# Kernel optimization log

Hardware: AMD Instinct MI355X
Metric: run time of the kernel (lower is better)

Reference implementation:

```python
import jax, jax.numpy as jnp
import numpy as np

HEADS = 8
DIM_HEAD = 64
DIM = 512
HIDDEN = HEADS * DIM_HEAD  # 512


def setup_inputs() -> dict:
    key = jax.random.key(0)
    k1, k2, k3, k4 = jax.random.split(key, 4)
    b, m, n = 4, 8, 512
    x = jax.random.normal(k1, (b, m, n, DIM), dtype=jnp.float32)
    pos_bias = jax.random.normal(k2, (HEADS, n, 16, 16), dtype=jnp.float32)
    # torch nn.Linear(dim, 3*hidden) weight is [3*hidden, dim]; we store the
    # transposed matmul form [dim, 3*hidden] for y = x @ W.
    w_qkv = jax.random.normal(k3, (DIM, 3 * HIDDEN), dtype=jnp.float32) * (DIM ** -0.5)
    w_out = jax.random.normal(k4, (HIDDEN, DIM), dtype=jnp.float32) * (HIDDEN ** -0.5)
    return {"x": x, "pos_bias": pos_bias, "w_qkv": w_qkv, "w_out": w_out}


def reference(x, pos_bias, w_qkv, w_out):
    b, m, n, _ = x.shape
    h, d = HEADS, DIM_HEAD
    scale = d ** -0.5
    qkv = jnp.einsum('bmnc,ce->bmne', x, w_qkv)  # [b,m,n,3*hidden]
    q, k, v = jnp.split(qkv, 3, axis=-1)
    # 'b m n (h d) -> (b m) h n d'
    def to_heads(t):
        return t.reshape(b * m, n, h, d).transpose(0, 2, 1, 3)
    q, k, v = to_heads(q), to_heads(k), to_heads(v)
    q = q * scale
    sim = jnp.einsum('bhid,bhjd->bhij', q, k)  # [(b*m), h, n, n]
    # pos_bias [h, n, p, q] -> mean over last two dims -> [h, n] -> broadcast [1,h,n,1]
    pb = pos_bias.mean(axis=(-2, -1))[None, :, :, None]
    sim = sim + pb
    sim = sim - jax.lax.stop_gradient(jnp.max(sim, axis=-1, keepdims=True))
    attn = jax.nn.softmax(sim, axis=-1)
    out = jnp.einsum('bhij,bhjd->bhid', attn, v)  # [(b*m), h, n, d]
    # '(b m) h n d -> b m n (h d)'
    out = out.transpose(0, 2, 1, 3).reshape(b, m, n, h * d)
    return jnp.einsum('bmne,ec->bmnc', out, w_out)
```

## Files before the change

### kernel.cpp

```cpp
#include <hip/hip_runtime.h>
#include <stdint.h>


typedef __attribute__((ext_vector_type(8))) short bf16x8;
typedef __attribute__((ext_vector_type(4))) float f32x4;
typedef __attribute__((ext_vector_type(4))) unsigned short us4;
typedef __attribute__((ext_vector_type(4))) float float4v;

__device__ __forceinline__ unsigned short f2b(float f) {
  union { float f; uint32_t u; } x; x.f = f;
  uint32_t r = x.u + 0x7fffu + ((x.u >> 16) & 1u);
  return (unsigned short)(r >> 16);
}

__device__ __forceinline__ uint32_t cvtpk(float lo, float hi) {
  uint32_t r;
  asm("v_cvt_pk_bf16_f32 %0, %1, %2" : "=v"(r) : "v"(lo), "v"(hi));
  return r;
}

__device__ __forceinline__ f32x4 mfma16(bf16x8 a, bf16x8 b, f32x4 c) {
  return __builtin_amdgcn_mfma_f32_16x16x32_bf16(a, b, c, 0, 0, 0);
}

__device__ __forceinline__ void gload_lds16(const unsigned short* g, unsigned short* l) {
  __builtin_amdgcn_global_load_lds(
      (const __attribute__((address_space(1))) unsigned int*)g,
      (__attribute__((address_space(3))) unsigned int*)l, 16, 0, 0);
}

__global__ __launch_bounds__(256) void cast_x_kernel(
    const float* __restrict__ src, unsigned short* __restrict__ dst) {
  size_t i = ((size_t)blockIdx.x * 256 + threadIdx.x) * 4;
  float4v v = *(const float4v*)(src + i);
  us4 o;
#pragma unroll
  for (int j = 0; j < 4; ++j) o[j] = f2b(v[j]);
  *(us4*)(dst + i) = o;
}

__global__ __launch_bounds__(256) void transpose_cast_kernel(
    const float* __restrict__ src, unsigned short* __restrict__ dst, int R, int C) {
  __shared__ float tile[64][65];
  const int tc0 = blockIdx.x * 64;
  const int tr0 = blockIdx.y * 64;
#pragma unroll
  for (int k2 = 0; k2 < 16; ++k2) {
    int idx = threadIdx.x + k2 * 256;
    int r = idx >> 6, c = idx & 63;
    tile[r][c] = src[(size_t)(tr0 + r) * C + tc0 + c];
  }
  __syncthreads();
#pragma unroll
  for (int k2 = 0; k2 < 16; ++k2) {
    int idx = threadIdx.x + k2 * 256;
    int c = idx >> 6, r = idx & 63;
    dst[(size_t)(tc0 + c) * R + tr0 + r] = f2b(tile[r][c]);
  }
}

__device__ __forceinline__ void gemm_core(
    const unsigned short* __restrict__ A, const unsigned short* __restrict__ Bt,
    int K, int r0, int c0, unsigned short* As, unsigned short* Bs,
    f32x4 (&acc)[4][4]) {
  const int tid = threadIdx.x;
  const int lane = tid & 63;
  const int wave = tid >> 6;
  const int wr = (wave >> 1) * 64;
  const int wc = (wave & 1) * 64;
  const int l15 = lane & 15;
  const int g = lane >> 4;
  const int lsw = l15 & 7;

#pragma unroll
  for (int m = 0; m < 4; ++m)
#pragma unroll
    for (int n = 0; n < 4; ++n) acc[m][n] = (f32x4){0.f, 0.f, 0.f, 0.f};

  for (int kt = 0; kt < K; kt += 64) {
#pragma unroll
    for (int i = 0; i < 4; ++i) {
      int chunk = tid + i * 256;
      int row = chunk >> 3;
      int csw = (chunk & 7) ^ (row & 7);
      gload_lds16(A + (size_t)(r0 + row) * K + kt + csw * 8, As + chunk * 8);
      gload_lds16(Bt + (size_t)(c0 + row) * K + kt + csw * 8, Bs + chunk * 8);
    }
    __syncthreads();
#pragma unroll
    for (int ks = 0; ks < 2; ++ks) {
      bf16x8 af[4], bfr[4];
      const int j = g + ks * 4;
      const int cj = (j ^ lsw) * 8;
#pragma unroll
      for (int m = 0; m < 4; ++m)
        af[m] = *(const bf16x8*)(As + (wr + m * 16 + l15) * 64 + cj);
#pragma unroll
      for (int n = 0; n < 4; ++n)
        bfr[n] = *(const bf16x8*)(Bs + (wc + n * 16 + l15) * 64 + cj);
#pragma unroll
      for (int m = 0; m < 4; ++m)
#pragma unroll
        for (int n = 0; n < 4; ++n) acc[m][n] = mfma16(af[m], bfr[n], acc[m][n]);
    }
    __syncthreads();
  }
}

__global__ __launch_bounds__(256) void gemm_qkv_kernel(
    const unsigned short* __restrict__ xb, const unsigned short* __restrict__ wqbT,
    unsigned short* __restrict__ qb, unsigned short* __restrict__ kb,
    unsigned short* __restrict__ vtb) {
  __shared__ unsigned short smem[16384];
  f32x4 acc[4][4];
  const int r0 = blockIdx.x * 128;
  const int c0 = blockIdx.y * 128;
  gemm_core(xb, wqbT, 512, r0, c0, smem, smem + 8192, acc);

  const int tid = threadIdx.x, lane = tid & 63, wave = tid >> 6;
  const int wr = (wave >> 1) * 64, wc = (wave & 1) * 64;
  const int l15 = lane & 15, g = lane >> 4;
  const int part = c0 >> 9;
  const float scl = (part == 0) ? 0.125f : 1.0f;

  if (part < 2) {
#pragma unroll
    for (int m = 0; m < 4; ++m) {
      int rbase = wr + m * 16 + 4 * g;
#pragma unroll
      for (int n = 0; n < 4; ++n) {
        int c = wc + n * 16 + l15;
        int c2 = c >> 3, ci = c & 7;
#pragma unroll
        for (int rr = 0; rr < 4; ++rr) {
          int r = rbase + rr;
          smem[r * 128 + ((c2 ^ (r & 15)) << 3) + ci] = f2b(acc[m][n][rr] * scl);
        }
      }
    }
    __syncthreads();
    unsigned short* dstb = (part == 0) ? qb : kb;
#pragma unroll
    for (int it = 0; it < 8; ++it) {
      int idx = tid + it * 256;
      int r = idx >> 4, c2 = idx & 15;
      bf16x8 v = *(const bf16x8*)(smem + r * 128 + ((c2 ^ (r & 15)) << 3));
      int e = c0 + c2 * 8;
      int rem = e & 511, h = rem >> 6, d = rem & 63;
      int ig = r0 + r;
      int bh = (ig >> 9) * 8 + h, i = ig & 511;
      *(bf16x8*)(dstb + ((size_t)bh * 512 + i) * 64 + d) = v;
    }
  } else {
#pragma unroll
    for (int m = 0; m < 4; ++m) {
      int rbase = wr + m * 16 + 4 * g;
      int r2 = rbase >> 3, rhalf = rbase & 7;
#pragma unroll
      for (int n = 0; n < 4; ++n) {
        int c = wc + n * 16 + l15;
        us4 v;
#pragma unroll
        for (int rr = 0; rr < 4; ++rr) v[rr] = f2b(acc[m][n][rr]);
        *(us4*)(smem + c * 128 + ((r2 ^ (c & 15)) << 3) + rhalf) = v;
      }
    }
    __syncthreads();
#pragma unroll
    for (int it = 0; it < 8; ++it) {
      int idx = tid + it * 256;
      int c = idx >> 4, r8 = idx & 15;
      bf16x8 v = *(const bf16x8*)(smem + c * 128 + ((r8 ^ (c & 15)) << 3));
      int e = c0 + c;
      int rem = e & 511, h = rem >> 6, d = rem & 63;
      int ig0 = r0 + r8 * 8;
      int bh = (ig0 >> 9) * 8 + h, i = ig0 & 511;
      *(bf16x8*)(vtb + ((size_t)bh * 64 + d) * 512 + i) = v;
    }
  }
}

__global__ __launch_bounds__(256) void gemm_out_kernel(
    const unsigned short* __restrict__ ao, const unsigned short* __restrict__ wobT,
    float* __restrict__ out) {
  __shared__ unsigned short smem[16384];
  f32x4 acc[4][4];
  const int r0 = blockIdx.x * 128;
  const int c0 = blockIdx.y * 128;
  gemm_core(ao, wobT, 512, r0, c0, smem, smem + 8192, acc);

  const int tid = threadIdx.x, lane = tid & 63, wave = tid >> 6;
  const int wr = (wave >> 1) * 64, wc = (wave & 1) * 64;
  const int l15 = lane & 15, g = lane >> 4;
#pragma unroll
  for (int m = 0; m < 4; ++m) {
    int i0g = r0 + wr + m * 16 + 4 * g;
#pragma unroll
    for (int n = 0; n < 4; ++n) {
      int e = c0 + wc + n * 16 + l15;
#pragma unroll
      for (int rr = 0; rr < 4; ++rr)
        out[(size_t)(i0g + rr) * 512 + e] = acc[m][n][rr];
    }
  }
}

__global__ __launch_bounds__(512, 4) void attn_kernel(
    const unsigned short* __restrict__ qb, const unsigned short* __restrict__ kb,
    const unsigned short* __restrict__ vtb, unsigned short* __restrict__ ao) {
  __shared__ unsigned short kbuf[2][8192];
  __shared__ unsigned short vbuf[2][8192];
  __shared__ unsigned short Ps[8][16][40];
  const int bh = blockIdx.x;
  const int qt = blockIdx.y;
  const int tid = threadIdx.x, lane = tid & 63, wave = tid >> 6;
  const int l15 = lane & 15, g = lane >> 4;
  const int qrow0 = qt * 128 + wave * 16;

  const unsigned short* Q = qb + ((size_t)bh * 512 + qrow0) * 64;
  const unsigned short* Kp = kb + (size_t)bh * 512 * 64;
  const unsigned short* Vt = vtb + (size_t)bh * 64 * 512;

  bf16x8 qf0 = *(const bf16x8*)(Q + l15 * 64 + g * 8);
  bf16x8 qf1 = *(const bf16x8*)(Q + l15 * 64 + 32 + g * 8);

  const int krow = tid >> 3;
  const int kck = (tid & 7) ^ (krow & 7);
  const int vrow = tid >> 4;
  const int vck = (tid & 15) ^ (vrow & 15);

  auto stage = [&](int t, int b) {
    const unsigned short* ks = Kp + ((size_t)t * 128 + krow) * 64 + kck * 8;
    gload_lds16(ks, kbuf[b] + tid * 8);
    gload_lds16(ks + 64 * 64, kbuf[b] + tid * 8 + 4096);
    const unsigned short* vs = Vt + (size_t)vrow * 512 + t * 128 + vck * 8;
    gload_lds16(vs, vbuf[b] + tid * 8);
    gload_lds16(vs + 32 * 512, vbuf[b] + tid * 8 + 4096);
  };

  f32x4 oacc[4];
#pragma unroll
  for (int m = 0; m < 4; ++m) oacc[m] = (f32x4){0.f, 0.f, 0.f, 0.f};
  float srow[4] = {0.f, 0.f, 0.f, 0.f};

  stage(0, 0);
  asm volatile("s_waitcnt vmcnt(0)" ::: "memory");
  __builtin_amdgcn_s_barrier();

  int cur = 0;
#pragma unroll
  for (int t = 0; t < 4; ++t) {
    if (t < 3) stage(t + 1, cur ^ 1);

    const unsigned short* kb_ = kbuf[cur];
    f32x4 s[8];
    const int c0i = g ^ (l15 & 7);
    __builtin_amdgcn_s_setprio(1);
#pragma unroll
    for (int tt = 0; tt < 8; ++tt) {
      int row = tt * 16 + l15;
      bf16x8 b0 = *(const bf16x8*)(kb_ + (row * 8 + c0i) * 8);
      bf16x8 b1 = *(const bf16x8*)(kb_ + (row * 8 + (c0i ^ 4)) * 8);
      f32x4 c = (f32x4){0.f, 0.f, 0.f, 0.f};
      c = mfma16(qf0, b0, c);
      s[tt] = mfma16(qf1, b1, c);
    }
    __builtin_amdgcn_s_setprio(0);

#pragma unroll
    for (int tt = 0; tt < 8; ++tt)
#pragma unroll
      for (int rr = 0; rr < 4; ++rr) {
        float e = __expf(s[tt][rr]);
        s[tt][rr] = e;
        srow[rr] += e;
      }

    const unsigned short* vb_ = vbuf[cur];
#pragma unroll
    for (int cc = 0; cc < 4; ++cc) {
#pragma unroll
      for (int rr = 0; rr < 4; ++rr) {
        uint32_t pk = cvtpk(s[cc * 2][rr], s[cc * 2 + 1][rr]);
        Ps[wave][4 * g + rr][l15] = (unsigned short)pk;
        Ps[wave][4 * g + rr][16 + l15] = (unsigned short)(pk >> 16);
      }
      asm volatile("s_waitcnt lgkmcnt(0)" ::: "memory");
      bf16x8 pf = *(const bf16x8*)(&Ps[wave][l15][g * 8]);
      __builtin_amdgcn_s_setprio(1);
#pragma unroll
      for (int m = 0; m < 4; ++m) {
        int vr = m * 16 + l15;
        bf16x8 vf = *(const bf16x8*)(vb_ + (vr * 16 + ((cc * 4 + g) ^ l15)) * 8);
        oacc[m] = mfma16(vf, pf, oacc[m]);
      }
      __builtin_amdgcn_s_setprio(0);
    }

    if (t < 3) {
      asm volatile("s_waitcnt vmcnt(0)" ::: "memory");
      __builtin_amdgcn_s_barrier();
      cur ^= 1;
    }
  }

#pragma unroll
  for (int rr = 0; rr < 4; ++rr)
#pragma unroll
    for (int o = 1; o < 16; o <<= 1) srow[rr] += __shfl_xor(srow[rr], o);
  int srcl = (l15 >> 2) * 16;
  float t0 = __shfl(srow[0], srcl), t1 = __shfl(srow[1], srcl);
  float t2 = __shfl(srow[2], srcl), t3 = __shfl(srow[3], srcl);
  int rq = l15 & 3;
  float sq = rq == 0 ? t0 : rq == 1 ? t1 : rq == 2 ? t2 : t3;
  float invq = 1.0f / sq;

  const int hh = bh & 7, bm = bh >> 3;
  unsigned short* aorow = ao + ((size_t)bm * 512 + qrow0 + l15) * 512 + hh * 64;
#pragma unroll
  for (int m = 0; m < 4; ++m) {
    union { us4 u; uint32_t w[2]; } uv;
    uv.w[0] = cvtpk(oacc[m][0] * invq, oacc[m][1] * invq);
    uv.w[1] = cvtpk(oacc[m][2] * invq, oacc[m][3] * invq);
    *(us4*)(aorow + m * 16 + 4 * g) = uv.u;
  }
}

extern "C" void kernel_launch(void* const* d_in, const int* in_sizes, int n_in,
                              void* d_out, int out_size, void* d_ws, size_t ws_size,
                              hipStream_t stream) {
  const float* x = (const float*)d_in[0];
  const float* w_qkv = (const float*)d_in[2];
  const float* w_out = (const float*)d_in[3];
  float* out = (float*)d_out;

  char* ws = (char*)d_ws;
  const size_t SZ_XB = 16384ull * 512 * 2;
  const size_t SZ_WQ = 1536ull * 512 * 2;
  const size_t SZ_WO = 512ull * 512 * 2;
  const size_t SZ_HB = 256ull * 512 * 64 * 2;
  unsigned short* xb = (unsigned short*)(ws);
  unsigned short* wqbT = (unsigned short*)(ws + SZ_XB);
  unsigned short* wobT = (unsigned short*)(ws + SZ_XB + SZ_WQ);
  unsigned short* qb = (unsigned short*)(ws + SZ_XB + SZ_WQ + SZ_WO);
  unsigned short* kb = (unsigned short*)(ws + SZ_XB + SZ_WQ + SZ_WO + SZ_HB);
  unsigned short* vtb = (unsigned short*)(ws + SZ_XB + SZ_WQ + SZ_WO + 2 * SZ_HB);
  unsigned short* ao = (unsigned short*)(ws + SZ_XB + SZ_WQ + SZ_WO + 3 * SZ_HB);

  cast_x_kernel<<<8192, 256, 0, stream>>>(x, xb);
  transpose_cast_kernel<<<dim3(1536 / 64, 512 / 64), 256, 0, stream>>>(w_qkv, wqbT, 512, 1536);
  transpose_cast_kernel<<<dim3(512 / 64, 512 / 64), 256, 0, stream>>>(w_out, wobT, 512, 512);
  gemm_qkv_kernel<<<dim3(128, 12), 256, 0, stream>>>(xb, wqbT, qb, kb, vtb);
  attn_kernel<<<dim3(256, 4), 512, 0, stream>>>(qb, kb, vtb, ao);
  gemm_out_kernel<<<dim3(128, 4), 256, 0, stream>>>(ao, wobT, out);
}
```

Measured before the change: 104.0 us.

## Double-buffer LDS tiles in GEMM core to overlap global loads with MFMA

The shared GEMM core now keeps two LDS stages per operand and issues the direct-to-LDS loads for the next K-tile before computing on the current one. This replaces the two syncthreads per iteration with a single waitcnt plus barrier. MFMA sections are wrapped in s_setprio to raise wave priority during compute. LDS use for the QKV and output GEMMs doubles to 64KB, which may cut occupancy. The wait also sits right after compute, so the amount of overlap is limited.

```diff
diff --git a/kernel.cpp b/kernel.cpp
--- a/kernel.cpp
+++ b/kernel.cpp
@@ -77,16 +77,29 @@
 #pragma unroll
     for (int n = 0; n < 4; ++n) acc[m][n] = (f32x4){0.f, 0.f, 0.f, 0.f};
 
-  for (int kt = 0; kt < K; kt += 64) {
+  auto stage = [&](int kt, int b) {
 #pragma unroll
     for (int i = 0; i < 4; ++i) {
       int chunk = tid + i * 256;
       int row = chunk >> 3;
       int csw = (chunk & 7) ^ (row & 7);
-      gload_lds16(A + (size_t)(r0 + row) * K + kt + csw * 8, As + chunk * 8);
-      gload_lds16(Bt + (size_t)(c0 + row) * K + kt + csw * 8, Bs + chunk * 8);
-    }
-    __syncthreads();
+      gload_lds16(A + (size_t)(r0 + row) * K + kt + csw * 8,
+                  As + b * 8192 + chunk * 8);
+      gload_lds16(Bt + (size_t)(c0 + row) * K + kt + csw * 8,
+                  Bs + b * 8192 + chunk * 8);
+    }
+  };
+
+  stage(0, 0);
+  asm volatile("s_waitcnt vmcnt(0)" ::: "memory");
+  __builtin_amdgcn_s_barrier();
+
+  const int NT = K >> 6;
+  int cur = 0;
+  for (int t = 0; t < NT; ++t) {
+    if (t + 1 < NT) stage((t + 1) << 6, cur ^ 1);
+    const unsigned short* as = As + cur * 8192;
+    const unsigned short* bs = Bs + cur * 8192;
 #pragma unroll
     for (int ks = 0; ks < 2; ++ks) {
       bf16x8 af[4], bfr[4];
@@ -94,28 +107,35 @@
       const int cj = (j ^ lsw) * 8;
 #pragma unroll
       for (int m = 0; m < 4; ++m)
-        af[m] = *(const bf16x8*)(As + (wr + m * 16 + l15) * 64 + cj);
+        af[m] = *(const bf16x8*)(as + (wr + m * 16 + l15) * 64 + cj);
 #pragma unroll
       for (int n = 0; n < 4; ++n)
-        bfr[n] = *(const bf16x8*)(Bs + (wc + n * 16 + l15) * 64 + cj);
+        bfr[n] = *(const bf16x8*)(bs + (wc + n * 16 + l15) * 64 + cj);
+      __builtin_amdgcn_s_setprio(1);
 #pragma unroll
       for (int m = 0; m < 4; ++m)
 #pragma unroll
         for (int n = 0; n < 4; ++n) acc[m][n] = mfma16(af[m], bfr[n], acc[m][n]);
-    }
-    __syncthreads();
-  }
+      __builtin_amdgcn_s_setprio(0);
+    }
+    if (t + 1 < NT) {
+      asm volatile("s_waitcnt vmcnt(0)" ::: "memory");
+      __builtin_amdgcn_s_barrier();
+      cur ^= 1;
+    }
+  }
+  __syncthreads();
 }
 
 __global__ __launch_bounds__(256) void gemm_qkv_kernel(
     const unsigned short* __restrict__ xb, const unsigned short* __restrict__ wqbT,
     unsigned short* __restrict__ qb, unsigned short* __restrict__ kb,
     unsigned short* __restrict__ vtb) {
-  __shared__ unsigned short smem[16384];
+  __shared__ unsigned short smem[32768];
   f32x4 acc[4][4];
   const int r0 = blockIdx.x * 128;
   const int c0 = blockIdx.y * 128;
-  gemm_core(xb, wqbT, 512, r0, c0, smem, smem + 8192, acc);
+  gemm_core(xb, wqbT, 512, r0, c0, smem, smem + 16384, acc);
 
   const int tid = threadIdx.x, lane = tid & 63, wave = tid >> 6;
   const int wr = (wave >> 1) * 64, wc = (wave & 1) * 64;
@@ -183,11 +203,11 @@
 __global__ __launch_bounds__(256) void gemm_out_kernel(
     const unsigned short* __restrict__ ao, const unsigned short* __restrict__ wobT,
     float* __restrict__ out) {
-  __shared__ unsigned short smem[16384];
+  __shared__ unsigned short smem[32768];
   f32x4 acc[4][4];
   const int r0 = blockIdx.x * 128;
   const int c0 = blockIdx.y * 128;
-  gemm_core(ao, wobT, 512, r0, c0, smem, smem + 8192, acc);
+  gemm_core(ao, wobT, 512, r0, c0, smem, smem + 16384, acc);
 
   const int tid = threadIdx.x, lane = tid & 63, wave = tid >> 6;
   const int wr = (wave >> 1) * 64, wc = (wave & 1) * 64;
```

Result: faster. 94.03 us (-9.6%).
